# Kernel optimization log

Measured on AMD Instinct MI355X. Metric: run time of the kernel, lower is better.

## Reference

```python
import jax, jax.numpy as jnp
import numpy as np

IN_FEATURES = 512
OUT_FEATURES = 512
GRID_SIZE = 8
SPLINE_ORDER = 3


def make_grid():
    # grid has grid_size + 2*spline_order + 1 knots in [-1, 1]
    return jnp.linspace(-1.0, 1.0, GRID_SIZE + 2 * SPLINE_ORDER + 1, dtype=jnp.float32)


def b_splines(x, grid):
    # x: (N, in)  ->  bases: (N, in, grid_size + spline_order)
    x = jnp.clip(x, -2.0, 2.0)[..., None]  # (N, in, 1)
    bases = ((x >= grid[:-1]) & (x < grid[1:])).astype(x.dtype)
    for k in range(1, SPLINE_ORDER + 1):
        denom1 = grid[k:-1] - grid[:-(k + 1)]
        denom1 = jnp.where(jnp.abs(denom1) < 1e-8, jnp.ones_like(denom1), denom1)
        denom2 = grid[k + 1:] - grid[1:-k]
        denom2 = jnp.where(jnp.abs(denom2) < 1e-8, jnp.ones_like(denom2), denom2)
        bases = ((x - grid[:-(k + 1)]) / denom1 * bases[..., :-1]
                 + (grid[k + 1:] - x) / denom2 * bases[..., 1:])
    return bases


def setup_inputs() -> dict:
    key = jax.random.key(0)
    kx, kb, ks = jax.random.split(key, 3)
    x = jax.random.normal(kx, (8192, IN_FEATURES), dtype=jnp.float32)
    # xavier_uniform with gain=0.5 for base_weight
    limit = 0.5 * np.sqrt(6.0 / (IN_FEATURES + OUT_FEATURES))
    base_weight = jax.random.uniform(kb, (OUT_FEATURES, IN_FEATURES), dtype=jnp.float32,
                                     minval=-limit, maxval=limit)
    spline_weight = 0.01 * jax.random.normal(
        ks, (OUT_FEATURES, IN_FEATURES, GRID_SIZE + SPLINE_ORDER), dtype=jnp.float32)
    return {"x": x, "base_weight": base_weight, "spline_weight": spline_weight}


def reference(x, base_weight, spline_weight):
    grid = make_grid()
    base_out = x @ base_weight.T                      # (N, out)
    basis = b_splines(x, grid)                        # (N, in, G+K)
    spline_out = jnp.einsum('bij,oij->bo', basis, spline_weight)
    return base_out + spline_out
```

## Files before the change

kernel.cpp:

```cpp
#include <hip/hip_runtime.h>
#include <stdint.h>

#define IN_F 512
#define OUT_F 512
#define NROWS 8192
#define NSLOT 12
#define KTOT (IN_F * NSLOT)
#define K16S (KTOT / 16)
#define SW_ROW (IN_F * 11)
#define KC_PAD 776
#define AROW 120

typedef __bf16 bf16x8 __attribute__((ext_vector_type(8)));
typedef __bf16 bf16x2 __attribute__((ext_vector_type(2)));
typedef float f32x16 __attribute__((ext_vector_type(16)));

__device__ ushort g_Wb[(K16S * 16 + 1) * 512];

__device__ __forceinline__ ushort f2bf(float f) {
    uint32_t u = __builtin_bit_cast(uint32_t, f);
    u += 0x7FFFu + ((u >> 16) & 1u);
    return (ushort)(u >> 16);
}

__global__ __launch_bounds__(256) void prep_weights(const float* __restrict__ bw,
                                                    const float* __restrict__ sw,
                                                    float* __restrict__ out) {
    __shared__ __align__(16) ushort kcol[4 * KC_PAD];
    const int t  = threadIdx.x;
    const int b  = blockIdx.x;
    const int nt = b & 15;
    const int kg = (b >> 4) & 7;
    const int hq = b >> 7;
    const int hv = hq >> 2;
    const int qr = hq & 3;
    const int o0 = nt * 32 + hv * 16 + qr * 4;
    const int f0 = kg * 64;

    {
        float4* o4 = (float4*)out;
        const float4 z = make_float4(0.f, 0.f, 0.f, 0.f);
        #pragma unroll
        for (int i = 0; i < 4; ++i) o4[(size_t)b * 1024 + i * 256 + t] = z;
    }

    {
        const int o_l = t >> 6;
        const int tr  = t & 63;
        const float* swr = sw + (size_t)(o0 + o_l) * SW_ROW + (size_t)f0 * 11;
        #pragma unroll
        for (int i = 0; i < 3; ++i) {
            int p4 = tr + i * 64;
            if (p4 < 176) {
                float4 v = ((const float4*)swr)[p4];
                uint pos = (uint)p4 * 4;
                #pragma unroll
                for (int c = 0; c < 4; ++c) {
                    uint pc = pos + c;
                    uint fl = pc / 11u;
                    uint j  = pc - fl * 11u;
                    float val = (c == 0) ? v.x : (c == 1) ? v.y : (c == 2) ? v.z : v.w;
                    kcol[o_l * KC_PAD + fl * NSLOT + j] = f2bf(val);
                }
            }
        }
        kcol[o_l * KC_PAD + tr * NSLOT + 11] =
            f2bf(bw[(size_t)(o0 + o_l) * IN_F + f0 + tr]);
    }
    __syncthreads();

    {
        const int ol4 = t & 3;
        const int ch  = t >> 2;
        #pragma unroll
        for (int i = 0; i < 2; ++i) {
            int idx = ch + i * 64;
            if (idx < 96) {
                int k16l = idx >> 1;
                int hf   = idx & 1;
                uint4 val = *(const uint4*)&kcol[ol4 * KC_PAD + k16l * 16 + hf * 8];
                ((uint4*)g_Wb)[((size_t)nt * K16S + kg * 48 + k16l) * 64
                               + hf * 32 + hv * 16 + qr * 4 + ol4] = val;
            }
        }
    }
}

__device__ __forceinline__ void eval12(float xx, uint p[6]) {
    float wpos = (xx + 1.0f) * 7.0f;
    float fi = floorf(wpos);
    int   i  = (int)fi;
    float u  = wpos - fi;
    bool inr = (xx >= -1.0f) && (xx < 1.0f);
    int   q  = i - 3;
    float um = 1.0f - u;
    float uu = u * u, u3 = uu * u;
    const float C6 = 1.0f / 6.0f;
    float s0 = (inr && q >= 0) ? C6 : 0.0f;
    float s1 = (inr && q >= -1 && q <= 9) ? C6 : 0.0f;
    float s2 = (inr && q >= -2 && q <= 8) ? C6 : 0.0f;
    float s3 = (inr && q <= 7) ? C6 : 0.0f;
    float b0 = um * um * um * s0;
    float b1 = fmaf(3.0f, u3, fmaf(-6.0f, uu, 4.0f)) * s1;
    float b2 = fmaf(-3.0f, u3, fmaf(3.0f, uu, fmaf(3.0f, u, 1.0f))) * s2;
    float b3 = u3 * s3;
    bf16x2 k01; k01[0] = (__bf16)b0; k01[1] = (__bf16)b1;
    bf16x2 k23; k23[0] = (__bf16)b2; k23[1] = (__bf16)b3;
    uint K01 = __builtin_bit_cast(uint, k01);
    uint K23 = __builtin_bit_cast(uint, k23);
    int r  = q & 1;
    int e0 = q & ~1;
    uint P0 = r ? (K01 << 16) : K01;
    uint P1 = r ? ((K01 >> 16) | (K23 << 16)) : K23;
    uint P2 = r ? (K23 >> 16) : 0u;
    #pragma unroll
    for (int pi = 0; pi < 6; ++pi) {
        int d = 2 * pi - e0;
        p[pi] = (d == 0) ? P0 : (d == 2) ? P1 : (d == 4) ? P2 : 0u;
    }
    p[5] = (p[5] & 0xFFFFu) | ((uint)f2bf(xx) << 16);
}

__device__ __forceinline__ void stage4(float4 xv, ushort* dst) {
    uint p[4][6];
    eval12(xv.x, p[0]);
    eval12(xv.y, p[1]);
    eval12(xv.z, p[2]);
    eval12(xv.w, p[3]);
    #pragma unroll
    for (int c = 0; c < 4; ++c) {
        uint2 w0; w0.x = p[c][0]; w0.y = p[c][1];
        uint2 w1; w1.x = p[c][2]; w1.y = p[c][3];
        uint2 w2; w2.x = p[c][4]; w2.y = p[c][5];
        *(uint2*)&dst[c * 12 + 0] = w0;
        *(uint2*)&dst[c * 12 + 4] = w1;
        *(uint2*)&dst[c * 12 + 8] = w2;
    }
}

__global__ __launch_bounds__(256, 3) void kan_gemm(const float* __restrict__ x,
                                                   float* __restrict__ out) {
    __shared__ __align__(16) ushort As[128 * AROW];

    const int t    = threadIdx.x;
    const int lane = t & 63;
    const int wv   = t >> 6;
    const int wr   = wv >> 1;
    const int wc   = wv & 1;
    const int ln31 = lane & 31;
    const int half = lane >> 5;

    const int bx = blockIdx.x;
    const int mb = bx >> 4;
    const int cg = (bx >> 2) & 3;
    const int kp = bx & 3;
    const int row_base = mb * 128;

    const int srow = t >> 1;
    const int fq   = t & 1;
    const float* xp = x + (size_t)(row_base + srow) * IN_F + kp * 128 + fq * 4;
    ushort* const sb = &As[srow * AROW + fq * 48];

    const int ntg0 = cg * 4 + wc * 2;
    const uint4* Bp0 = (const uint4*)g_Wb + (size_t)ntg0 * K16S * 64 + lane;
    const uint4* Bp1 = Bp0 + (size_t)K16S * 64;

    f32x16 acc[2][2] = {};

    float4 xv = *(const float4*)xp;

    #pragma unroll 1
    for (int gi = 0; gi < 16; ++gi) {
        const int g = kp * 16 + gi;
        uint4 breg[6][2];
        #pragma unroll
        for (int ks = 0; ks < 6; ++ks) {
            breg[ks][0] = Bp0[(size_t)(g * 6 + ks) * 64];
            breg[ks][1] = Bp1[(size_t)(g * 6 + ks) * 64];
        }
        const int gn = (gi + 1 < 16) ? gi + 1 : gi;
        float4 xn = *(const float4*)(xp + gn * 8);

        __syncthreads();
        stage4(xv, sb);
        __syncthreads();

        #pragma unroll
        for (int ks = 0; ks < 6; ++ks) {
            uint4 a0 = *(const uint4*)&As[(wr * 64 + ln31) * AROW + ks * 16 + half * 8];
            uint4 a1 = *(const uint4*)&As[(wr * 64 + 32 + ln31) * AROW + ks * 16 + half * 8];
            bf16x8 af0 = __builtin_bit_cast(bf16x8, a0);
            bf16x8 af1 = __builtin_bit_cast(bf16x8, a1);
            bf16x8 bf0 = __builtin_bit_cast(bf16x8, breg[ks][0]);
            bf16x8 bf1 = __builtin_bit_cast(bf16x8, breg[ks][1]);
            acc[0][0] = __builtin_amdgcn_mfma_f32_32x32x16_bf16(af0, bf0, acc[0][0], 0, 0, 0);
            acc[0][1] = __builtin_amdgcn_mfma_f32_32x32x16_bf16(af0, bf1, acc[0][1], 0, 0, 0);
            acc[1][0] = __builtin_amdgcn_mfma_f32_32x32x16_bf16(af1, bf0, acc[1][0], 0, 0, 0);
            acc[1][1] = __builtin_amdgcn_mfma_f32_32x32x16_bf16(af1, bf1, acc[1][1], 0, 0, 0);
        }
        xv = xn;
    }

    #pragma unroll
    for (int mt = 0; mt < 2; ++mt) {
        #pragma unroll
        for (int nt2 = 0; nt2 < 2; ++nt2) {
            int rb = row_base + wr * 64 + mt * 32 + 4 * half;
            int cc = cg * 128 + wc * 64 + nt2 * 32 + ln31;
            #pragma unroll
            for (int reg = 0; reg < 16; ++reg) {
                int rr = rb + (reg & 3) + 8 * (reg >> 2);
                unsafeAtomicAdd(&out[(size_t)rr * OUT_F + cc], acc[mt][nt2][reg]);
            }
        }
    }
}

extern "C" void kernel_launch(void* const* d_in, const int* in_sizes, int n_in,
                              void* d_out, int out_size, void* d_ws, size_t ws_size,
                              hipStream_t stream) {
    const float* x  = (const float*)d_in[0];
    const float* bw = (const float*)d_in[1];
    const float* sw = (const float*)d_in[2];
    float* out = (float*)d_out;
    hipLaunchKernelGGL(prep_weights, dim3(1024), dim3(256), 0, stream, bw, sw, out);
    hipLaunchKernelGGL(kan_gemm, dim3(1024), dim3(256), 0, stream, x, out);
}
```

Baseline: 165.4 us.

## Double-buffer spline-basis LDS tile and overlap staging with MFMA

The A-tile in shared memory is now double-buffered. Each iteration evaluates the next chunk's B-spline basis into the alternate buffer while the MFMAs consume the current one, so one of the two barriers per iteration goes away. MFMA sections are wrapped in s_setprio to favour matrix issue. The doubled LDS footprint lowers the occupancy hint from 3 to 2 blocks per CU, which reduces latency hiding across waves.

```diff
diff --git a/kernel.cpp b/kernel.cpp
--- a/kernel.cpp
+++ b/kernel.cpp
@@ -10,6 +10,7 @@
 #define SW_ROW (IN_F * 11)
 #define KC_PAD 776
 #define AROW 120
+#define ABUF (128 * AROW)
 
 typedef __bf16 bf16x8 __attribute__((ext_vector_type(8)));
 typedef __bf16 bf16x2 __attribute__((ext_vector_type(2)));
@@ -138,9 +139,9 @@
     }
 }
 
-__global__ __launch_bounds__(256, 3) void kan_gemm(const float* __restrict__ x,
+__global__ __launch_bounds__(256, 2) void kan_gemm(const float* __restrict__ x,
                                                    float* __restrict__ out) {
-    __shared__ __align__(16) ushort As[128 * AROW];
+    __shared__ __align__(16) ushort As[2 * ABUF];
 
     const int t    = threadIdx.x;
     const int lane = t & 63;
@@ -159,36 +160,46 @@
     const int srow = t >> 1;
     const int fq   = t & 1;
     const float* xp = x + (size_t)(row_base + srow) * IN_F + kp * 128 + fq * 4;
-    ushort* const sb = &As[srow * AROW + fq * 48];
+    const int sboff = srow * AROW + fq * 48;
 
     const int ntg0 = cg * 4 + wc * 2;
-    const uint4* Bp0 = (const uint4*)g_Wb + (size_t)ntg0 * K16S * 64 + lane;
-    const uint4* Bp1 = Bp0 + (size_t)K16S * 64;
+    const uint4* Bc0 = (const uint4*)g_Wb + (size_t)ntg0 * K16S * 64 + lane
+                       + (size_t)(kp * 16) * 6 * 64;
+    const uint4* Bc1 = Bc0 + (size_t)K16S * 64;
+
+    const int aoff0 = (wr * 64 + ln31) * AROW + half * 8;
+    const int aoff1 = (wr * 64 + 32 + ln31) * AROW + half * 8;
 
     f32x16 acc[2][2] = {};
 
     float4 xv = *(const float4*)xp;
+    stage4(xv, &As[sboff]);
+    xv = *(const float4*)(xp + 8);
+    __syncthreads();
 
     #pragma unroll 1
     for (int gi = 0; gi < 16; ++gi) {
-        const int g = kp * 16 + gi;
         uint4 breg[6][2];
         #pragma unroll
         for (int ks = 0; ks < 6; ++ks) {
-            breg[ks][0] = Bp0[(size_t)(g * 6 + ks) * 64];
-            breg[ks][1] = Bp1[(size_t)(g * 6 + ks) * 64];
-        }
-        const int gn = (gi + 1 < 16) ? gi + 1 : gi;
-        float4 xn = *(const float4*)(xp + gn * 8);
-
-        __syncthreads();
-        stage4(xv, sb);
-        __syncthreads();
-
+            breg[ks][0] = Bc0[ks * 64];
+            breg[ks][1] = Bc1[ks * 64];
+        }
+        Bc0 += 6 * 64;
+        Bc1 += 6 * 64;
+
+        const int cur = (gi & 1) ? ABUF : 0;
+        const int nxt = (gi & 1) ? 0 : ABUF;
+
+        if (gi < 15) stage4(xv, &As[nxt + sboff]);
+        const int gn = (gi + 2 < 16) ? gi + 2 : 14;
+        xv = *(const float4*)(xp + gn * 8);
+
+        __builtin_amdgcn_s_setprio(1);
         #pragma unroll
         for (int ks = 0; ks < 6; ++ks) {
-            uint4 a0 = *(const uint4*)&As[(wr * 64 + ln31) * AROW + ks * 16 + half * 8];
-            uint4 a1 = *(const uint4*)&As[(wr * 64 + 32 + ln31) * AROW + ks * 16 + half * 8];
+            uint4 a0 = *(const uint4*)&As[cur + aoff0 + ks * 16];
+            uint4 a1 = *(const uint4*)&As[cur + aoff1 + ks * 16];
             bf16x8 af0 = __builtin_bit_cast(bf16x8, a0);
             bf16x8 af1 = __builtin_bit_cast(bf16x8, a1);
             bf16x8 bf0 = __builtin_bit_cast(bf16x8, breg[ks][0]);
@@ -198,7 +209,8 @@
             acc[1][0] = __builtin_amdgcn_mfma_f32_32x32x16_bf16(af1, bf0, acc[1][0], 0, 0, 0);
             acc[1][1] = __builtin_amdgcn_mfma_f32_32x32x16_bf16(af1, bf1, acc[1][1], 0, 0, 0);
         }
-        xv = xn;
+        __builtin_amdgcn_s_setprio(0);
+        __syncthreads();
     }
 
     #pragma unroll
```

After: 183.6 us. 11.0% more time.

## Widen GEMM blocks to 512 threads covering 256 columns and split B loads

Applied to the files above, without the earlier changes.

Each block now has 8 waves covering 128 rows by 256 output columns, so one staged B-spline A tile in shared memory feeds twice as many columns. This halves the redundant basis evaluation per block, and each thread now evaluates 2 features instead of 4. Half of the B-fragment loads are now issued after the staging barriers, and the MFMA section runs at raised wave priority through s_setprio. The trade-offs are fewer blocks (512), larger blocks, and a different occupancy target that may increase register pressure.

```diff
diff --git a/kernel.cpp b/kernel.cpp
--- a/kernel.cpp
+++ b/kernel.cpp
@@ -121,14 +121,12 @@
     p[5] = (p[5] & 0xFFFFu) | ((uint)f2bf(xx) << 16);
 }
 
-__device__ __forceinline__ void stage4(float4 xv, ushort* dst) {
-    uint p[4][6];
+__device__ __forceinline__ void stage2(float2 xv, ushort* dst) {
+    uint p[2][6];
     eval12(xv.x, p[0]);
     eval12(xv.y, p[1]);
-    eval12(xv.z, p[2]);
-    eval12(xv.w, p[3]);
     #pragma unroll
-    for (int c = 0; c < 4; ++c) {
+    for (int c = 0; c < 2; ++c) {
         uint2 w0; w0.x = p[c][0]; w0.y = p[c][1];
         uint2 w1; w1.x = p[c][2]; w1.y = p[c][3];
         uint2 w2; w2.x = p[c][4]; w2.y = p[c][5];
@@ -138,66 +136,91 @@
     }
 }
 
-__global__ __launch_bounds__(256, 3) void kan_gemm(const float* __restrict__ x,
+__global__ __launch_bounds__(512, 4) void kan_gemm(const float* __restrict__ x,
                                                    float* __restrict__ out) {
     __shared__ __align__(16) ushort As[128 * AROW];
 
     const int t    = threadIdx.x;
     const int lane = t & 63;
     const int wv   = t >> 6;
-    const int wr   = wv >> 1;
-    const int wc   = wv & 1;
+    const int wr   = wv >> 2;
+    const int wc   = wv & 3;
     const int ln31 = lane & 31;
     const int half = lane >> 5;
 
     const int bx = blockIdx.x;
-    const int mb = bx >> 4;
-    const int cg = (bx >> 2) & 3;
+    const int mb = bx >> 3;
+    const int cg2 = (bx >> 2) & 1;
     const int kp = bx & 3;
     const int row_base = mb * 128;
 
-    const int srow = t >> 1;
-    const int fq   = t & 1;
-    const float* xp = x + (size_t)(row_base + srow) * IN_F + kp * 128 + fq * 4;
-    ushort* const sb = &As[srow * AROW + fq * 48];
-
-    const int ntg0 = cg * 4 + wc * 2;
+    const int srow = t >> 2;
+    const int fq   = t & 3;
+    const float* xp = x + (size_t)(row_base + srow) * IN_F + kp * 128 + fq * 2;
+    ushort* const sb = &As[srow * AROW + fq * 24];
+
+    const int ntg0 = cg2 * 8 + wc * 2;
     const uint4* Bp0 = (const uint4*)g_Wb + (size_t)ntg0 * K16S * 64 + lane;
     const uint4* Bp1 = Bp0 + (size_t)K16S * 64;
 
+    const int aoff0 = (wr * 64 + ln31) * AROW + half * 8;
+    const int aoff1 = (wr * 64 + 32 + ln31) * AROW + half * 8;
+
     f32x16 acc[2][2] = {};
 
-    float4 xv = *(const float4*)xp;
+    float2 xv = *(const float2*)xp;
 
     #pragma unroll 1
     for (int gi = 0; gi < 16; ++gi) {
         const int g = kp * 16 + gi;
-        uint4 breg[6][2];
-        #pragma unroll
-        for (int ks = 0; ks < 6; ++ks) {
-            breg[ks][0] = Bp0[(size_t)(g * 6 + ks) * 64];
-            breg[ks][1] = Bp1[(size_t)(g * 6 + ks) * 64];
+        uint4 bregA[3][2];
+        #pragma unroll
+        for (int ks = 0; ks < 3; ++ks) {
+            bregA[ks][0] = Bp0[(size_t)(g * 6 + ks) * 64];
+            bregA[ks][1] = Bp1[(size_t)(g * 6 + ks) * 64];
         }
         const int gn = (gi + 1 < 16) ? gi + 1 : gi;
-        float4 xn = *(const float4*)(xp + gn * 8);
+        float2 xn = *(const float2*)(xp + gn * 8);
 
         __syncthreads();
-        stage4(xv, sb);
+        stage2(xv, sb);
         __syncthreads();
 
-        #pragma unroll
-        for (int ks = 0; ks < 6; ++ks) {
-            uint4 a0 = *(const uint4*)&As[(wr * 64 + ln31) * AROW + ks * 16 + half * 8];
-            uint4 a1 = *(const uint4*)&As[(wr * 64 + 32 + ln31) * AROW + ks * 16 + half * 8];
+        uint4 bregB[3][2];
+        #pragma unroll
+        for (int ks = 0; ks < 3; ++ks) {
+            bregB[ks][0] = Bp0[(size_t)(g * 6 + 3 + ks) * 64];
+            bregB[ks][1] = Bp1[(size_t)(g * 6 + 3 + ks) * 64];
+        }
+
+        __builtin_amdgcn_s_setprio(1);
+        #pragma unroll
+        for (int ks = 0; ks < 3; ++ks) {
+            uint4 a0 = *(const uint4*)&As[aoff0 + ks * 16];
+            uint4 a1 = *(const uint4*)&As[aoff1 + ks * 16];
             bf16x8 af0 = __builtin_bit_cast(bf16x8, a0);
             bf16x8 af1 = __builtin_bit_cast(bf16x8, a1);
-            bf16x8 bf0 = __builtin_bit_cast(bf16x8, breg[ks][0]);
-            bf16x8 bf1 = __builtin_bit_cast(bf16x8, breg[ks][1]);
+            bf16x8 bf0 = __builtin_bit_cast(bf16x8, bregA[ks][0]);
+            bf16x8 bf1 = __builtin_bit_cast(bf16x8, bregA[ks][1]);
             acc[0][0] = __builtin_amdgcn_mfma_f32_32x32x16_bf16(af0, bf0, acc[0][0], 0, 0, 0);
             acc[0][1] = __builtin_amdgcn_mfma_f32_32x32x16_bf16(af0, bf1, acc[0][1], 0, 0, 0);
             acc[1][0] = __builtin_amdgcn_mfma_f32_32x32x16_bf16(af1, bf0, acc[1][0], 0, 0, 0);
             acc[1][1] = __builtin_amdgcn_mfma_f32_32x32x16_bf16(af1, bf1, acc[1][1], 0, 0, 0);
         }
+        #pragma unroll
+        for (int ks = 0; ks < 3; ++ks) {
+            uint4 a0 = *(const uint4*)&As[aoff0 + (ks + 3) * 16];
+            uint4 a1 = *(const uint4*)&As[aoff1 + (ks + 3) * 16];
+            bf16x8 af0 = __builtin_bit_cast(bf16x8, a0);
+            bf16x8 af1 = __builtin_bit_cast(bf16x8, a1);
+            bf16x8 bf0 = __builtin_bit_cast(bf16x8, bregB[ks][0]);
+            bf16x8 bf1 = __builtin_bit_cast(bf16x8, bregB[ks][1]);
+            acc[0][0] = __builtin_amdgcn_mfma_f32_32x32x16_bf16(af0, bf0, acc[0][0], 0, 0, 0);
+            acc[0][1] = __builtin_amdgcn_mfma_f32_32x32x16_bf16(af0, bf1, acc[0][1], 0, 0, 0);
+            acc[1][0] = __builtin_amdgcn_mfma_f32_32x32x16_bf16(af1, bf0, acc[1][0], 0, 0, 0);
+            acc[1][1] = __builtin_amdgcn_mfma_f32_32x32x16_bf16(af1, bf1, acc[1][1], 0, 0, 0);
+        }
+        __builtin_amdgcn_s_setprio(0);
         xv = xn;
     }
 
@@ -206,7 +229,7 @@
         #pragma unroll
         for (int nt2 = 0; nt2 < 2; ++nt2) {
             int rb = row_base + wr * 64 + mt * 32 + 4 * half;
-            int cc = cg * 128 + wc * 64 + nt2 * 32 + ln31;
+            int cc = cg2 * 256 + wc * 64 + nt2 * 32 + ln31;
             #pragma unroll
             for (int reg = 0; reg < 16; ++reg) {
                 int rr = rb + (reg & 3) + 8 * (reg >> 2);
@@ -224,5 +247,5 @@
     const float* sw = (const float*)d_in[2];
     float* out = (float*)d_out;
     hipLaunchKernelGGL(prep_weights, dim3(1024), dim3(256), 0, stream, bw, sw, out);
-    hipLaunchKernelGGL(kan_gemm, dim3(1024), dim3(256), 0, stream, x, out);
-}
+    hipLaunchKernelGGL(kan_gemm, dim3(512), dim3(512), 0, stream, x, out);
+}
```

After: 168.4 us. Within noise of the previous version (+1.8%).
